# Kernel optimization log

Measured on AMD Instinct MI355X. Metric: run time of the kernel, lower is better.

The kernel has to match this reference:

```python
import jax, jax.numpy as jnp
import numpy as np

B, S, D, H = 8, 128, 256, 8
T = S + 1
HD = D // H  # head_dim = 32
GAMMA = 1.0
NEG_INF = -1e9
LN_EPS = 1e-5


def setup_inputs() -> dict:
    key = jax.random.key(0)
    ks = jax.random.split(key, 16)
    sc = 0.05
    return {
        "desc_embeddings": jax.random.normal(ks[0], (B, S, D), jnp.float32),
        "name_value_embeddings": jax.random.normal(ks[1], (B, T, D), jnp.float32),
        "prior_Q": jax.random.uniform(ks[2], (B, H, S, S), jnp.float32),
        "Wq": jax.random.normal(ks[3], (D, D), jnp.float32) * sc,
        "bq": jnp.zeros((D,), jnp.float32),
        "Wk": jax.random.normal(ks[4], (D, D), jnp.float32) * sc,
        "bk": jnp.zeros((D,), jnp.float32),
        "Wv": jax.random.normal(ks[5], (D, D), jnp.float32) * sc,
        "bv": jnp.zeros((D,), jnp.float32),
        "wa": jax.random.normal(ks[6], (3 * HD,), jnp.float32) * sc,  # attn_proj weight (out=1)
        "ba": jnp.zeros((), jnp.float32),
        "We1": jax.random.normal(ks[7], (2 * D, D), jnp.float32) * sc,
        "be1": jnp.zeros((D,), jnp.float32),
        "ln_g": jnp.ones((D,), jnp.float32),
        "ln_b": jnp.zeros((D,), jnp.float32),
        "We2": jax.random.normal(ks[8], (D, D), jnp.float32) * sc,
        "be2": jnp.zeros((D,), jnp.float32),
    }


def _layer_norm(x, g, b):
    mu = jnp.mean(x, axis=-1, keepdims=True)
    var = jnp.mean(jnp.square(x - mu), axis=-1, keepdims=True)
    return (x - mu) * jax.lax.rsqrt(var + LN_EPS) * g + b


def _heads(x, W, b):  # [B,T,D] -> [B,H,T,HD]
    return (x @ W + b).reshape(B, T, H, HD).transpose(0, 2, 1, 3)


def reference(desc_embeddings, name_value_embeddings, prior_Q,
              Wq, bq, Wk, bk, Wv, bv, wa, ba,
              We1, be1, ln_g, ln_b, We2, be2):
    # structural adjacency (same for every batch element): CLS->Var on, Var->CLS off,
    # Var-Var fully connected without self-loops
    adj = jnp.zeros((T, T), jnp.float32)
    adj = adj.at[1:, 1:].set(1.0 - jnp.eye(S, dtype=jnp.float32))
    adj = adj.at[0, 1:].set(1.0)

    q = _heads(name_value_embeddings, Wq, bq)  # [B,H,T,HD]
    k = _heads(name_value_embeddings, Wk, bk)
    v = _heads(name_value_embeddings, Wv, bv)

    # edge attributes: pairwise concat of desc embeddings, CLS rows/cols use [desc,desc]
    desc = desc_embeddings
    var_edge = jnp.concatenate([
        jnp.broadcast_to(desc[:, :, None, :], (B, S, S, D)),
        jnp.broadcast_to(desc[:, None, :, :], (B, S, S, D)),
    ], axis=-1)  # [B,S,S,2D]
    cls_edge = jnp.concatenate([desc, desc], axis=-1)  # [B,S,2D]
    edge = jnp.zeros((B, T, T, 2 * D), jnp.float32)
    edge = edge.at[:, 1:, 1:].set(var_edge)
    edge = edge.at[:, 0, 1:].set(cls_edge)
    edge = edge.at[:, 1:, 0].set(cls_edge)

    # edge_update MLP: Linear(2D->D) -> LayerNorm -> ReLU -> Linear(D->D)
    h = jax.nn.relu(_layer_norm(edge @ We1 + be1, ln_g, ln_b)) @ We2 + be2  # [B,T,T,D]
    # split into heads, mask by adjacency: [B,H,T,T,HD]
    edge_h = h.reshape(B, T, T, H, HD).transpose(0, 3, 1, 2, 4)
    edge_h = edge_h * adj[None, None, :, :, None]

    # gat_v1 + attn_proj(cat[q_i, k_j, e_ij]) is linear -> decompose to avoid
    # materializing the [B,H,T,T,3*HD] concat
    wa_q, wa_k, wa_e = wa[:HD], wa[HD:2 * HD], wa[2 * HD:]
    logits = (jnp.einsum('bhid,d->bhi', q, wa_q)[:, :, :, None]
              + jnp.einsum('bhjd,d->bhj', k, wa_k)[:, :, None, :]
              + jnp.einsum('bhijd,d->bhij', edge_h, wa_e)
              + ba)  # [B,H,T,T]

    # prior_Q logit-bias injection on Var-Var block
    eps = 1e-6
    p = jnp.clip(prior_Q, eps, 1.0 - eps)
    bias = (jnp.log(p) - jnp.log(1.0 - p)) * GAMMA  # [B,H,S,S]
    logits = logits.at[:, :, 1:, 1:].add(bias)

    # structural mask as pre-softmax -inf
    logits = logits + (adj == 0).astype(logits.dtype)[None, None] * NEG_INF

    attn = jax.nn.softmax(logits, axis=-1)  # [B,H,T,T]
    ctx = jnp.einsum('bhij,bhjd->bhid', attn, v)  # [B,H,T,HD]
    basis_outputs = ctx.transpose(0, 2, 1, 3)  # [B,T,H,HD]
    return basis_outputs, attn
```

## Files before the change

### kernel.cpp

```cpp
#include <hip/hip_runtime.h>
#include <math.h>

#define B 8
#define S 128
#define D 256
#define H 8
#define T 129
#define HD 32
#define BT (B*T)
#define NEG_INF -1000000000.0f
#define LN_EPS 1e-5f

__global__ __launch_bounds__(256) void prep_w(
    const float* __restrict__ Wq, const float* __restrict__ bq,
    const float* __restrict__ Wk, const float* __restrict__ bk,
    const float* __restrict__ We2, const float* __restrict__ be2,
    const float* __restrict__ wa,
    float* __restrict__ Wqk, float* __restrict__ bqk,
    float* __restrict__ W2aT, float* __restrict__ econst)
{
    int id = blockIdx.x * 256 + threadIdx.x;
    if (id < 2048) {
        int c = id >> 3, h = id & 7;
        float s = 0.f;
        #pragma unroll
        for (int d = 0; d < HD; ++d) s = fmaf(Wq[c*D + h*HD + d], wa[d], s);
        Wqk[c*16 + h] = s;
    } else if (id < 4096) {
        int id2 = id - 2048; int c = id2 >> 3, h = id2 & 7;
        float s = 0.f;
        #pragma unroll
        for (int d = 0; d < HD; ++d) s = fmaf(Wk[c*D + h*HD + d], wa[HD + d], s);
        Wqk[c*16 + 8 + h] = s;
    } else if (id < 6144) {
        int id2 = id - 4096; int h = id2 / D, c = id2 % D;
        float s = 0.f;
        #pragma unroll
        for (int d = 0; d < HD; ++d) s = fmaf(We2[c*D + h*HD + d], wa[2*HD + d], s);
        W2aT[h*D + c] = s;
    } else if (id < 6152) {
        int h = id - 6144;
        float s = 0.f;
        #pragma unroll
        for (int d = 0; d < HD; ++d) s = fmaf(bq[h*HD + d], wa[d], s);
        bqk[h] = s;
    } else if (id < 6160) {
        int h = id - 6152;
        float s = 0.f;
        #pragma unroll
        for (int d = 0; d < HD; ++d) s = fmaf(bk[h*HD + d], wa[HD + d], s);
        bqk[8 + h] = s;
    } else if (id < 6168) {
        int h = id - 6160;
        float s = 0.f;
        #pragma unroll
        for (int d = 0; d < HD; ++d) s = fmaf(be2[h*HD + d], wa[2*HD + d], s);
        econst[h] = s;
    }
}

__global__ __launch_bounds__(256) void gemm3(
    const float* __restrict__ nv, const float* __restrict__ desc,
    const float* __restrict__ Wv, const float* __restrict__ bv,
    const float* __restrict__ We1, const float* __restrict__ be1,
    const float* __restrict__ Wqk, const float* __restrict__ bqk,
    float* __restrict__ v, float* __restrict__ U, float* __restrict__ V,
    float* __restrict__ sU, float* __restrict__ sV, float* __restrict__ qdkdT)
{
    const int which = blockIdx.y;
    const int tid = threadIdx.x;
    __shared__ float xs[16][D];
    __shared__ float psum[4][8];

    if (which == 3) {
        if (blockIdx.x >= 65) return;
        const int r0 = blockIdx.x * 16;
        const int r = tid >> 4, c = tid & 15;
        for (int t = tid; t < 16 * D; t += 256) {
            int rr = r0 + (t >> 8);
            xs[t >> 8][t & 255] = (rr < BT) ? nv[rr * D + (t & 255)] : 0.f;
        }
        __syncthreads();
        float acc = 0.f;
        for (int kk = 0; kk < D; kk += 4) {
            float4 x = *(const float4*)&xs[r][kk];
            acc = fmaf(x.x, Wqk[(kk+0)*16 + c], acc);
            acc = fmaf(x.y, Wqk[(kk+1)*16 + c], acc);
            acc = fmaf(x.z, Wqk[(kk+2)*16 + c], acc);
            acc = fmaf(x.w, Wqk[(kk+3)*16 + c], acc);
        }
        const int rr = r0 + r;
        if (rr < BT) qdkdT[c*BT + rr] = acc + bqk[c];
        return;
    }

    const float* X; const float* W; const float* bias; float* out; int rows;
    if (which == 0)      { X = nv;   W = Wv;        bias = bv;  out = v; rows = BT; }
    else if (which == 1) { X = desc; W = We1;       bias = be1; out = U; rows = B*S; }
    else                 { X = desc; W = We1 + D*D; bias = nullptr; out = V; rows = B*S; }

    const int r0 = blockIdx.x * 8;
    if (r0 >= rows) return;

    #pragma unroll
    for (int r = 0; r < 8; ++r) {
        int rr = r0 + r;
        xs[r][tid] = (rr < rows) ? X[rr * D + tid] : 0.f;
    }
    __syncthreads();

    float acc[8] = {0.f,0.f,0.f,0.f,0.f,0.f,0.f,0.f};
    for (int kk = 0; kk < D; kk += 4) {
        float w0 = W[(kk+0)*D + tid];
        float w1 = W[(kk+1)*D + tid];
        float w2 = W[(kk+2)*D + tid];
        float w3 = W[(kk+3)*D + tid];
        #pragma unroll
        for (int r = 0; r < 8; ++r) {
            float4 x = *(const float4*)&xs[r][kk];
            acc[r] = fmaf(x.x, w0, acc[r]);
            acc[r] = fmaf(x.y, w1, acc[r]);
            acc[r] = fmaf(x.z, w2, acc[r]);
            acc[r] = fmaf(x.w, w3, acc[r]);
        }
    }
    const float bb = bias ? bias[tid] : 0.f;
    #pragma unroll
    for (int r = 0; r < 8; ++r) {
        int rr = r0 + r;
        if (rr < rows) out[rr * D + tid] = acc[r] + bb;
    }

    if (which >= 1) {
        const int wv = tid >> 6, ln = tid & 63;
        #pragma unroll
        for (int r = 0; r < 8; ++r) {
            float sps = acc[r] + bb;
            #pragma unroll
            for (int m = 32; m >= 1; m >>= 1) sps += __shfl_xor(sps, m);
            if (ln == 0) psum[wv][r] = sps;
        }
        __syncthreads();
        if (tid < 8) {
            float* dst = (which == 1) ? sU : sV;
            dst[r0 + tid] = psum[0][tid] + psum[1][tid] + psum[2][tid] + psum[3][tid];
        }
    }
}

__device__ __forceinline__ float head_reduce(float* ph, int lane) {
    {
        const bool hi = (lane & 1);
        float k0 = hi ? ph[4] : ph[0], d0 = hi ? ph[0] : ph[4];
        float k1 = hi ? ph[5] : ph[1], d1 = hi ? ph[1] : ph[5];
        float k2 = hi ? ph[6] : ph[2], d2 = hi ? ph[2] : ph[6];
        float k3 = hi ? ph[7] : ph[3], d3 = hi ? ph[3] : ph[7];
        ph[0] = k0 + __shfl_xor(d0, 1);
        ph[1] = k1 + __shfl_xor(d1, 1);
        ph[2] = k2 + __shfl_xor(d2, 1);
        ph[3] = k3 + __shfl_xor(d3, 1);
    }
    {
        const bool hi = (lane & 2);
        float k0 = hi ? ph[2] : ph[0], d0 = hi ? ph[0] : ph[2];
        float k1 = hi ? ph[3] : ph[1], d1 = hi ? ph[1] : ph[3];
        ph[0] = k0 + __shfl_xor(d0, 2);
        ph[1] = k1 + __shfl_xor(d1, 2);
    }
    {
        const bool hi = (lane & 4);
        float k0 = hi ? ph[1] : ph[0], d0 = hi ? ph[0] : ph[1];
        ph[0] = k0 + __shfl_xor(d0, 4);
    }
    float r = ph[0];
    r += __shfl_xor(r, 8);
    r += __shfl_xor(r, 16);
    r += __shfl_xor(r, 32);
    return r;
}

__global__ __launch_bounds__(512, 4) void edge_attn(
    const float* __restrict__ U, const float* __restrict__ V,
    const float* __restrict__ W2aT, const float* __restrict__ econst,
    const float* __restrict__ ln_g, const float* __restrict__ ln_b,
    const float* __restrict__ qdkdT, const float* __restrict__ prior,
    const float* __restrict__ v, const float* __restrict__ ba,
    const float* __restrict__ sU, const float* __restrict__ sV,
    float* __restrict__ out_basis, float* __restrict__ out_attn)
{
    const int bid = blockIdx.x;
    const int b = bid / T, i = bid % T;
    const int tid = threadIdx.x, lane = tid & 63, wid = tid >> 6;
    const int c0 = lane * 4;

    __shared__ float escl[H][132];
    __shared__ float pat[H][132];

    const float4 g4 = *(const float4*)(ln_g + c0);
    const float4 b4 = *(const float4*)(ln_b + c0);
    float4 w[H];
    #pragma unroll
    for (int h = 0; h < H; ++h) w[h] = *(const float4*)(W2aT + h*D + c0);

    float4 u4i = make_float4(0.f, 0.f, 0.f, 0.f);
    float sUi = 0.f;
    if (i >= 1) {
        u4i = *(const float4*)(U + (size_t)(b*S + (i-1))*D + c0);
        sUi = sU[b*S + (i-1)];
    }

    const int hmap = 4*(lane&1) + 2*((lane>>1)&1) + ((lane>>2)&1);
    const float ecl = (lane < 8) ? econst[hmap] : 0.f;

    const int j0 = 1 + wid * 16;
    const float* Vb  = V  + (size_t)(b*S + (j0-1))*D + c0;
    const float* Ub  = U  + (size_t)(b*S + (j0-1))*D + c0;
    const float* sVb = sV + b*S + (j0-1);
    const float* sUb = sU + b*S + (j0-1);

    #pragma unroll 2
    for (int jj = 0; jj < 16; jj += 2) {
        const float4 va  = *(const float4*)(Vb + (size_t)jj*D);
        const float4 vb4 = *(const float4*)(Vb + (size_t)(jj+1)*D);
        float4 ua, ub; float su_a, su_b;
        if (i == 0) {
            ua = *(const float4*)(Ub + (size_t)jj*D);
            ub = *(const float4*)(Ub + (size_t)(jj+1)*D);
            su_a = sUb[jj]; su_b = sUb[jj+1];
        } else { ua = u4i; ub = u4i; su_a = sUi; su_b = sUi; }

        const float mua = (su_a + sVb[jj])   * (1.f/D);
        const float mub = (su_b + sVb[jj+1]) * (1.f/D);

        const float ya0 = ua.x + va.x,  ya1 = ua.y + va.y;
        const float ya2 = ua.z + va.z,  ya3 = ua.w + va.w;
        const float yb0 = ub.x + vb4.x, yb1 = ub.y + vb4.y;
        const float yb2 = ub.z + vb4.z, yb3 = ub.w + vb4.w;

        float s2a = fmaf(ya0, ya0, fmaf(ya1, ya1, fmaf(ya2, ya2, ya3 * ya3)));
        float s2b = fmaf(yb0, yb0, fmaf(yb1, yb1, fmaf(yb2, yb2, yb3 * yb3)));
        #pragma unroll
        for (int m = 32; m >= 1; m >>= 1) {
            s2a += __shfl_xor(s2a, m);
            s2b += __shfl_xor(s2b, m);
        }
        const float vara = fmaf(-mua, mua, s2a * (1.f/D));
        const float varb = fmaf(-mub, mub, s2b * (1.f/D));
        const float rsa = rsqrtf(vara + LN_EPS);
        const float rsb = rsqrtf(varb + LN_EPS);

        const float ta0 = fmaxf(fmaf((ya0 - mua) * rsa, g4.x, b4.x), 0.f);
        const float ta1 = fmaxf(fmaf((ya1 - mua) * rsa, g4.y, b4.y), 0.f);
        const float ta2 = fmaxf(fmaf((ya2 - mua) * rsa, g4.z, b4.z), 0.f);
        const float ta3 = fmaxf(fmaf((ya3 - mua) * rsa, g4.w, b4.w), 0.f);
        const float tb0 = fmaxf(fmaf((yb0 - mub) * rsb, g4.x, b4.x), 0.f);
        const float tb1 = fmaxf(fmaf((yb1 - mub) * rsb, g4.y, b4.y), 0.f);
        const float tb2 = fmaxf(fmaf((yb2 - mub) * rsb, g4.z, b4.z), 0.f);
        const float tb3 = fmaxf(fmaf((yb3 - mub) * rsb, g4.w, b4.w), 0.f);

        float pha[8], phb[8];
        #pragma unroll
        for (int h = 0; h < H; ++h) {
            pha[h] = fmaf(ta0, w[h].x, fmaf(ta1, w[h].y, fmaf(ta2, w[h].z, ta3 * w[h].w)));
            phb[h] = fmaf(tb0, w[h].x, fmaf(tb1, w[h].y, fmaf(tb2, w[h].z, tb3 * w[h].w)));
        }
        const float ra = head_reduce(pha, lane);
        const float rb = head_reduce(phb, lane);
        if (lane < 8) {
            escl[hmap][j0 + jj]     = ra + ecl;
            escl[hmap][j0 + jj + 1] = rb + ecl;
        }
    }
    __syncthreads();

    const int h = wid;
    const int bh = b*H + h;
    const float qdv = qdkdT[h*BT + b*T + i];
    const float ba0 = ba[0];
    const int j1 = 1 + lane, j2 = 65 + lane;
    const bool val1 = !(i >= 1 && j1 == i);
    const bool val2 = !(i >= 1 && j2 == i);
    const float* kT = qdkdT + (8 + h)*BT + b*T;

    float l1 = NEG_INF, l2 = NEG_INF;
    if (val1) {
        l1 = qdv + kT[j1] + escl[h][j1] + ba0;
        if (i >= 1) {
            float pr = prior[((size_t)bh*S + (i-1))*S + (j1-1)];
            pr = fminf(fmaxf(pr, 1e-6f), 1.f - 1e-6f);
            l1 += __logf(pr) - __logf(1.f - pr);
        }
    }
    if (val2) {
        l2 = qdv + kT[j2] + escl[h][j2] + ba0;
        if (i >= 1) {
            float pr = prior[((size_t)bh*S + (i-1))*S + (j2-1)];
            pr = fminf(fmaxf(pr, 1e-6f), 1.f - 1e-6f);
            l2 += __logf(pr) - __logf(1.f - pr);
        }
    }

    float m = fmaxf(l1, l2);
    #pragma unroll
    for (int mm = 32; mm >= 1; mm >>= 1) m = fmaxf(m, __shfl_xor(m, mm));
    const float e1 = val1 ? __expf(l1 - m) : 0.f;
    const float e2 = val2 ? __expf(l2 - m) : 0.f;
    float ssum = e1 + e2;
    #pragma unroll
    for (int mm = 32; mm >= 1; mm >>= 1) ssum += __shfl_xor(ssum, mm);
    const float inv = 1.f / ssum;
    const float a1 = e1 * inv, a2 = e2 * inv;

    float* arow = out_attn + (size_t)(bh*T + i)*T;
    arow[j1] = a1;
    arow[j2] = a2;
    if (lane == 0) arow[0] = 0.f;
    pat[h][j1] = a1;
    pat[h][j2] = a2;
    __syncthreads();

    const int dg = lane & 7;
    const int jg = lane >> 3;
    const float* vbase = v + (size_t)(b*T)*D + h*HD + dg*4;
    float4 acc4 = make_float4(0.f, 0.f, 0.f, 0.f);
    #pragma unroll
    for (int k = 0; k < 16; ++k) {
        const int j = 1 + jg*16 + k;
        const float p = pat[h][j];
        const float4 vv = *(const float4*)(vbase + (size_t)j*D);
        acc4.x = fmaf(p, vv.x, acc4.x);
        acc4.y = fmaf(p, vv.y, acc4.y);
        acc4.z = fmaf(p, vv.z, acc4.z);
        acc4.w = fmaf(p, vv.w, acc4.w);
    }
    #pragma unroll
    for (int mm = 8; mm <= 32; mm <<= 1) {
        acc4.x += __shfl_xor(acc4.x, mm);
        acc4.y += __shfl_xor(acc4.y, mm);
        acc4.z += __shfl_xor(acc4.z, mm);
        acc4.w += __shfl_xor(acc4.w, mm);
    }
    if (jg == 0)
        *(float4*)(out_basis + ((size_t)(b*T + i)*H + h)*HD + dg*4) = acc4;
}

extern "C" void kernel_launch(void* const* d_in, const int* in_sizes, int n_in,
                              void* d_out, int out_size, void* d_ws, size_t ws_size,
                              hipStream_t stream) {
    const float* desc  = (const float*)d_in[0];
    const float* nv    = (const float*)d_in[1];
    const float* prior = (const float*)d_in[2];
    const float* Wq  = (const float*)d_in[3];
    const float* bq  = (const float*)d_in[4];
    const float* Wk  = (const float*)d_in[5];
    const float* bk  = (const float*)d_in[6];
    const float* Wv  = (const float*)d_in[7];
    const float* bv  = (const float*)d_in[8];
    const float* wa  = (const float*)d_in[9];
    const float* ba  = (const float*)d_in[10];
    const float* We1 = (const float*)d_in[11];
    const float* be1 = (const float*)d_in[12];
    const float* lng = (const float*)d_in[13];
    const float* lnb = (const float*)d_in[14];
    const float* We2 = (const float*)d_in[15];
    const float* be2 = (const float*)d_in[16];

    float* ws = (float*)d_ws;
    float* U     = ws; ws += B*S*D;
    float* V     = ws; ws += B*S*D;
    float* v     = ws; ws += B*T*D;
    float* Wqk   = ws; ws += D*16;
    float* bqk   = ws; ws += 16;
    float* W2aT  = ws; ws += H*D;
    float* ec    = ws; ws += H;
    float* qdkdT = ws; ws += 16*BT;
    float* sU    = ws; ws += B*S;
    float* sV    = ws; ws += B*S;

    float* out_basis = (float*)d_out;
    float* out_attn  = out_basis + B*T*H*HD;

    prep_w<<<dim3(25), 256, 0, stream>>>(Wq, bq, Wk, bk, We2, be2, wa,
                                         Wqk, bqk, W2aT, ec);
    gemm3<<<dim3(129, 4), 256, 0, stream>>>(nv, desc, Wv, bv, We1, be1,
                                            Wqk, bqk, v, U, V, sU, sV, qdkdT);
    edge_attn<<<dim3(B*T), 512, 0, stream>>>(U, V, W2aT, ec, lng, lnb,
                                             qdkdT, prior, v, ba, sU, sV,
                                             out_basis, out_attn);
}
```

Measured before the change: 159.9 us.

## Precompute LayerNorm statistics via sum-of-squares decomposition instead of per-pair shuffle reductions

The edge kernel no longer runs a 64-lane shuffle reduction per (i,j) pair to get the LayerNorm variance. The GEMM kernel now also emits per-row sums of squares for U and V, and each edge block computes mean and rstd for all 128 pairs up front from one U·V dot product per pair, storing them in shared memory. The LN affine is folded into a single FMA per element, prior and k loads are hoisted before the edge loop, and the PV accumulation uses an interleaved j index. In exchange each block does an extra 256-wide dot product per pair plus a barrier, and the E[y²]-μ² form may lose some precision.

After: 176.8 us. 1.11x slower.

```diff
diff --git a/kernel.cpp b/kernel.cpp
--- a/kernel.cpp
+++ b/kernel.cpp
@@ -65,12 +65,15 @@
     const float* __restrict__ We1, const float* __restrict__ be1,
     const float* __restrict__ Wqk, const float* __restrict__ bqk,
     float* __restrict__ v, float* __restrict__ U, float* __restrict__ V,
-    float* __restrict__ sU, float* __restrict__ sV, float* __restrict__ qdkdT)
+    float* __restrict__ sU, float* __restrict__ sV,
+    float* __restrict__ s2U, float* __restrict__ s2V,
+    float* __restrict__ qdkdT)
 {
     const int which = blockIdx.y;
     const int tid = threadIdx.x;
     __shared__ float xs[16][D];
     __shared__ float psum[4][8];
+    __shared__ float psq[4][8];
 
     if (which == 3) {
         if (blockIdx.x >= 65) return;
@@ -135,15 +138,22 @@
         const int wv = tid >> 6, ln = tid & 63;
         #pragma unroll
         for (int r = 0; r < 8; ++r) {
-            float sps = acc[r] + bb;
+            float sval = acc[r] + bb;
+            float sps = sval;
+            float sq  = sval * sval;
             #pragma unroll
-            for (int m = 32; m >= 1; m >>= 1) sps += __shfl_xor(sps, m);
-            if (ln == 0) psum[wv][r] = sps;
+            for (int m = 32; m >= 1; m >>= 1) {
+                sps += __shfl_xor(sps, m);
+                sq  += __shfl_xor(sq,  m);
+            }
+            if (ln == 0) { psum[wv][r] = sps; psq[wv][r] = sq; }
         }
         __syncthreads();
         if (tid < 8) {
-            float* dst = (which == 1) ? sU : sV;
-            dst[r0 + tid] = psum[0][tid] + psum[1][tid] + psum[2][tid] + psum[3][tid];
+            float* d1 = (which == 1) ? sU  : sV;
+            float* d2 = (which == 1) ? s2U : s2V;
+            d1[r0 + tid] = psum[0][tid] + psum[1][tid] + psum[2][tid] + psum[3][tid];
+            d2[r0 + tid] = psq[0][tid]  + psq[1][tid]  + psq[2][tid]  + psq[3][tid];
         }
     }
 }
@@ -157,7 +167,7 @@
         float k3 = hi ? ph[7] : ph[3], d3 = hi ? ph[3] : ph[7];
         ph[0] = k0 + __shfl_xor(d0, 1);
         ph[1] = k1 + __shfl_xor(d1, 1);
-        ph[2] = k2 + __shfl_xor(d2, 1);
+        ph[2] = k2 + __shfl_xor(d2, 2 - 1);
         ph[3] = k3 + __shfl_xor(d3, 1);
     }
     {
@@ -186,6 +196,7 @@
     const float* __restrict__ qdkdT, const float* __restrict__ prior,
     const float* __restrict__ v, const float* __restrict__ ba,
     const float* __restrict__ sU, const float* __restrict__ sV,
+    const float* __restrict__ s2U, const float* __restrict__ s2V,
     float* __restrict__ out_basis, float* __restrict__ out_attn)
 {
     const int bid = blockIdx.x;
@@ -195,74 +206,106 @@
 
     __shared__ float escl[H][132];
     __shared__ float pat[H][132];
+    __shared__ float muS[132];
+    __shared__ float rsS[132];
+
+    const int h = wid;
+    const int bh = b*H + h;
+    const int j1 = 1 + lane, j2 = 65 + lane;
+    const float qdv = qdkdT[h*BT + b*T + i];
+    const float ba0 = ba[0];
+    const float* kT = qdkdT + (8 + h)*BT + b*T;
+    const float k1 = kT[j1], k2 = kT[j2];
+    float pr1 = 0.5f, pr2 = 0.5f;
+    if (i >= 1) {
+        pr1 = prior[((size_t)bh*S + (i-1))*S + (j1-1)];
+        pr2 = prior[((size_t)bh*S + (i-1))*S + (j2-1)];
+    }
+
+    {
+        const int jp = (tid >> 2) + 1;
+        const int part = tid & 3;
+        const int urowi = (i >= 1) ? (b*S + i - 1) : (b*S + jp - 1);
+        const float* urow = U + (size_t)urowi * D;
+        const float* vrow = V + (size_t)(b*S + jp - 1) * D;
+        float dotp = 0.f;
+        #pragma unroll
+        for (int c = 0; c < 64; c += 4) {
+            float4 uu = *(const float4*)(urow + part*64 + c);
+            float4 vv = *(const float4*)(vrow + part*64 + c);
+            dotp = fmaf(uu.x, vv.x, dotp);
+            dotp = fmaf(uu.y, vv.y, dotp);
+            dotp = fmaf(uu.z, vv.z, dotp);
+            dotp = fmaf(uu.w, vv.w, dotp);
+        }
+        dotp += __shfl_xor(dotp, 1);
+        dotp += __shfl_xor(dotp, 2);
+        if (part == 0) {
+            const float su  = sU[urowi];
+            const float s2u = s2U[urowi];
+            const float svj  = sV[b*S + jp - 1];
+            const float s2vj = s2V[b*S + jp - 1];
+            const float mu  = (su + svj) * (1.f/D);
+            const float var = fmaf(-mu, mu, (fmaf(2.f, dotp, s2u + s2vj)) * (1.f/D));
+            muS[jp] = mu;
+            rsS[jp] = rsqrtf(var + LN_EPS);
+        }
+    }
 
     const float4 g4 = *(const float4*)(ln_g + c0);
     const float4 b4 = *(const float4*)(ln_b + c0);
     float4 w[H];
     #pragma unroll
-    for (int h = 0; h < H; ++h) w[h] = *(const float4*)(W2aT + h*D + c0);
+    for (int hh = 0; hh < H; ++hh) w[hh] = *(const float4*)(W2aT + hh*D + c0);
 
     float4 u4i = make_float4(0.f, 0.f, 0.f, 0.f);
-    float sUi = 0.f;
-    if (i >= 1) {
-        u4i = *(const float4*)(U + (size_t)(b*S + (i-1))*D + c0);
-        sUi = sU[b*S + (i-1)];
-    }
+    if (i >= 1) u4i = *(const float4*)(U + (size_t)(b*S + (i-1))*D + c0);
 
     const int hmap = 4*(lane&1) + 2*((lane>>1)&1) + ((lane>>2)&1);
     const float ecl = (lane < 8) ? econst[hmap] : 0.f;
 
     const int j0 = 1 + wid * 16;
-    const float* Vb  = V  + (size_t)(b*S + (j0-1))*D + c0;
-    const float* Ub  = U  + (size_t)(b*S + (j0-1))*D + c0;
-    const float* sVb = sV + b*S + (j0-1);
-    const float* sUb = sU + b*S + (j0-1);
+    const float* Vb = V + (size_t)(b*S + (j0-1))*D + c0;
+    const float* Ub = U + (size_t)(b*S + (j0-1))*D + c0;
+
+    __syncthreads();
 
     #pragma unroll 2
     for (int jj = 0; jj < 16; jj += 2) {
         const float4 va  = *(const float4*)(Vb + (size_t)jj*D);
         const float4 vb4 = *(const float4*)(Vb + (size_t)(jj+1)*D);
-        float4 ua, ub; float su_a, su_b;
+        float4 ua, ub;
         if (i == 0) {
             ua = *(const float4*)(Ub + (size_t)jj*D);
             ub = *(const float4*)(Ub + (size_t)(jj+1)*D);
-            su_a = sUb[jj]; su_b = sUb[jj+1];
-        } else { ua = u4i; ub = u4i; su_a = sUi; su_b = sUi; }
-
-        const float mua = (su_a + sVb[jj])   * (1.f/D);
-        const float mub = (su_b + sVb[jj+1]) * (1.f/D);
-
-        const float ya0 = ua.x + va.x,  ya1 = ua.y + va.y;
-        const float ya2 = ua.z + va.z,  ya3 = ua.w + va.w;
-        const float yb0 = ub.x + vb4.x, yb1 = ub.y + vb4.y;
-        const float yb2 = ub.z + vb4.z, yb3 = ub.w + vb4.w;
-
-        float s2a = fmaf(ya0, ya0, fmaf(ya1, ya1, fmaf(ya2, ya2, ya3 * ya3)));
-        float s2b = fmaf(yb0, yb0, fmaf(yb1, yb1, fmaf(yb2, yb2, yb3 * yb3)));
-        #pragma unroll
-        for (int m = 32; m >= 1; m >>= 1) {
-            s2a += __shfl_xor(s2a, m);
-            s2b += __shfl_xor(s2b, m);
-        }
-        const float vara = fmaf(-mua, mua, s2a * (1.f/D));
-        const float varb = fmaf(-mub, mub, s2b * (1.f/D));
-        const float rsa = rsqrtf(vara + LN_EPS);
-        const float rsb = rsqrtf(varb + LN_EPS);
-
-        const float ta0 = fmaxf(fmaf((ya0 - mua) * rsa, g4.x, b4.x), 0.f);
-        const float ta1 = fmaxf(fmaf((ya1 - mua) * rsa, g4.y, b4.y), 0.f);
-        const float ta2 = fmaxf(fmaf((ya2 - mua) * rsa, g4.z, b4.z), 0.f);
-        const float ta3 = fmaxf(fmaf((ya3 - mua) * rsa, g4.w, b4.w), 0.f);
-        const float tb0 = fmaxf(fmaf((yb0 - mub) * rsb, g4.x, b4.x), 0.f);
-        const float tb1 = fmaxf(fmaf((yb1 - mub) * rsb, g4.y, b4.y), 0.f);
-        const float tb2 = fmaxf(fmaf((yb2 - mub) * rsb, g4.z, b4.z), 0.f);
-        const float tb3 = fmaxf(fmaf((yb3 - mub) * rsb, g4.w, b4.w), 0.f);
+        } else { ua = u4i; ub = u4i; }
+
+        const float mua = muS[j0 + jj],  rsa = rsS[j0 + jj];
+        const float mub = muS[j0 + jj + 1], rsb = rsS[j0 + jj + 1];
+
+        const float rga0 = rsa * g4.x, rga1 = rsa * g4.y;
+        const float rga2 = rsa * g4.z, rga3 = rsa * g4.w;
+        const float ofa0 = fmaf(-mua, rga0, b4.x), ofa1 = fmaf(-mua, rga1, b4.y);
+        const float ofa2 = fmaf(-mua, rga2, b4.z), ofa3 = fmaf(-mua, rga3, b4.w);
+        const float rgb0 = rsb * g4.x, rgb1 = rsb * g4.y;
+        const float rgb2 = rsb * g4.z, rgb3 = rsb * g4.w;
+        const float ofb0 = fmaf(-mub, rgb0, b4.x), ofb1 = fmaf(-mub, rgb1, b4.y);
+        const float ofb2 = fmaf(-mub, rgb2, b4.z), ofb3 = fmaf(-mub, rgb3, b4.w);
+
+        const float ta0 = fmaxf(fmaf(ua.x + va.x,  rga0, ofa0), 0.f);
+        const float ta1 = fmaxf(fmaf(ua.y + va.y,  rga1, ofa1), 0.f);
+        const float ta2 = fmaxf(fmaf(ua.z + va.z,  rga2, ofa2), 0.f);
+        const float ta3 = fmaxf(fmaf(ua.w + va.w,  rga3, ofa3), 0.f);
+        const float tb0 = fmaxf(fmaf(ub.x + vb4.x, rgb0, ofb0), 0.f);
+        const float tb1 = fmaxf(fmaf(ub.y + vb4.y, rgb1, ofb1), 0.f);
+        const float tb2 = fmaxf(fmaf(ub.z + vb4.z, rgb2, ofb2), 0.f);
+        const float tb3 = fmaxf(fmaf(ub.w + vb4.w, rgb3, ofb3), 0.f);
 
         float pha[8], phb[8];
         #pragma unroll
-        for (int h = 0; h < H; ++h) {
-            pha[h] = fmaf(ta0, w[h].x, fmaf(ta1, w[h].y, fmaf(ta2, w[h].z, ta3 * w[h].w)));
-            phb[h] = fmaf(tb0, w[h].x, fmaf(tb1, w[h].y, fmaf(tb2, w[h].z, tb3 * w[h].w)));
+        for (int hh = 0; hh < H; ++hh) {
+            pha[hh] = fmaf(ta0, w[hh].x, fmaf(ta1, w[hh].y, fmaf(ta2, w[hh].z, ta3 * w[hh].w)));
+            phb[hh] = fmaf(tb0, w[hh].x, fmaf(tb1, w[hh].y, fmaf(tb2, w[hh].z, tb3 * w[hh].w)));
         }
         const float ra = head_reduce(pha, lane);
         const float rb = head_reduce(phb, lane);
@@ -273,29 +316,21 @@
     }
     __syncthreads();
 
-    const int h = wid;
-    const int bh = b*H + h;
-    const float qdv = qdkdT[h*BT + b*T + i];
-    const float ba0 = ba[0];
-    const int j1 = 1 + lane, j2 = 65 + lane;
     const bool val1 = !(i >= 1 && j1 == i);
     const bool val2 = !(i >= 1 && j2 == i);
-    const float* kT = qdkdT + (8 + h)*BT + b*T;
 
     float l1 = NEG_INF, l2 = NEG_INF;
     if (val1) {
-        l1 = qdv + kT[j1] + escl[h][j1] + ba0;
+        l1 = qdv + k1 + escl[h][j1] + ba0;
         if (i >= 1) {
-            float pr = prior[((size_t)bh*S + (i-1))*S + (j1-1)];
-            pr = fminf(fmaxf(pr, 1e-6f), 1.f - 1e-6f);
+            float pr = fminf(fmaxf(pr1, 1e-6f), 1.f - 1e-6f);
             l1 += __logf(pr) - __logf(1.f - pr);
         }
     }
     if (val2) {
-        l2 = qdv + kT[j2] + escl[h][j2] + ba0;
+        l2 = qdv + k2 + escl[h][j2] + ba0;
         if (i >= 1) {
-            float pr = prior[((size_t)bh*S + (i-1))*S + (j2-1)];
-            pr = fminf(fmaxf(pr, 1e-6f), 1.f - 1e-6f);
+            float pr = fminf(fmaxf(pr2, 1e-6f), 1.f - 1e-6f);
             l2 += __logf(pr) - __logf(1.f - pr);
         }
     }
@@ -325,7 +360,7 @@
     float4 acc4 = make_float4(0.f, 0.f, 0.f, 0.f);
     #pragma unroll
     for (int k = 0; k < 16; ++k) {
-        const int j = 1 + jg*16 + k;
+        const int j = 1 + k*8 + jg;
         const float p = pat[h][j];
         const float4 vv = *(const float4*)(vbase + (size_t)j*D);
         acc4.x = fmaf(p, vv.x, acc4.x);
@@ -376,6 +411,8 @@
     float* qdkdT = ws; ws += 16*BT;
     float* sU    = ws; ws += B*S;
     float* sV    = ws; ws += B*S;
+    float* s2U   = ws; ws += B*S;
+    float* s2V   = ws; ws += B*S;
 
     float* out_basis = (float*)d_out;
     float* out_attn  = out_basis + B*T*H*HD;
@@ -383,8 +420,10 @@
     prep_w<<<dim3(25), 256, 0, stream>>>(Wq, bq, Wk, bk, We2, be2, wa,
                                          Wqk, bqk, W2aT, ec);
     gemm3<<<dim3(129, 4), 256, 0, stream>>>(nv, desc, Wv, bv, We1, be1,
-                                            Wqk, bqk, v, U, V, sU, sV, qdkdT);
+                                            Wqk, bqk, v, U, V,
+                                            sU, sV, s2U, s2V, qdkdT);
     edge_attn<<<dim3(B*T), 512, 0, stream>>>(U, V, W2aT, ec, lng, lnb,
-                                             qdkdT, prior, v, ba, sU, sV,
+                                             qdkdT, prior, v, ba,
+                                             sU, sV, s2U, s2V,
                                              out_basis, out_attn);
 }
```

## Batch four edges per wave with a transpose-style shuffle reduction and prefetch prior loads

Applied to the files above, without the earlier changes.

The edge loop in edge_attn now handles four j values per iteration. The LayerNorm variance and per-head projection sums for all four are folded into one butterfly transpose-reduction, so the wave issues far fewer cross-lane shuffles per edge. The prior, k and q loads for the softmax stage are hoisted to kernel start so their latency overlaps the edge computation. The PV loop now interleaves j indices across lane groups. The cost is more live registers per thread under launch_bounds(512,4), which could cause spills, and more complex lane-select logic.

Result: faster. 146.6 us (-8.3%).

```diff
diff --git a/kernel.cpp b/kernel.cpp
--- a/kernel.cpp
+++ b/kernel.cpp
@@ -146,37 +146,6 @@
             dst[r0 + tid] = psum[0][tid] + psum[1][tid] + psum[2][tid] + psum[3][tid];
         }
     }
-}
-
-__device__ __forceinline__ float head_reduce(float* ph, int lane) {
-    {
-        const bool hi = (lane & 1);
-        float k0 = hi ? ph[4] : ph[0], d0 = hi ? ph[0] : ph[4];
-        float k1 = hi ? ph[5] : ph[1], d1 = hi ? ph[1] : ph[5];
-        float k2 = hi ? ph[6] : ph[2], d2 = hi ? ph[2] : ph[6];
-        float k3 = hi ? ph[7] : ph[3], d3 = hi ? ph[3] : ph[7];
-        ph[0] = k0 + __shfl_xor(d0, 1);
-        ph[1] = k1 + __shfl_xor(d1, 1);
-        ph[2] = k2 + __shfl_xor(d2, 1);
-        ph[3] = k3 + __shfl_xor(d3, 1);
-    }
-    {
-        const bool hi = (lane & 2);
-        float k0 = hi ? ph[2] : ph[0], d0 = hi ? ph[0] : ph[2];
-        float k1 = hi ? ph[3] : ph[1], d1 = hi ? ph[1] : ph[3];
-        ph[0] = k0 + __shfl_xor(d0, 2);
-        ph[1] = k1 + __shfl_xor(d1, 2);
-    }
-    {
-        const bool hi = (lane & 4);
-        float k0 = hi ? ph[1] : ph[0], d0 = hi ? ph[0] : ph[1];
-        ph[0] = k0 + __shfl_xor(d0, 4);
-    }
-    float r = ph[0];
-    r += __shfl_xor(r, 8);
-    r += __shfl_xor(r, 16);
-    r += __shfl_xor(r, 32);
-    return r;
 }
 
 __global__ __launch_bounds__(512, 4) void edge_attn(
@@ -196,106 +165,161 @@
     __shared__ float escl[H][132];
     __shared__ float pat[H][132];
 
+    const int h = wid;
+    const int bh = b*H + h;
+    const int j1 = 1 + lane, j2 = 65 + lane;
+    const float qdv = qdkdT[h*BT + b*T + i];
+    const float ba0 = ba[0];
+    const float* kT = qdkdT + (8 + h)*BT + b*T;
+    const float k1 = kT[j1], k2 = kT[j2];
+    float pr1 = 0.5f, pr2 = 0.5f;
+    if (i >= 1) {
+        pr1 = prior[((size_t)bh*S + (i-1))*S + (j1-1)];
+        pr2 = prior[((size_t)bh*S + (i-1))*S + (j2-1)];
+    }
+
     const float4 g4 = *(const float4*)(ln_g + c0);
     const float4 b4 = *(const float4*)(ln_b + c0);
     float4 w[H];
     #pragma unroll
-    for (int h = 0; h < H; ++h) w[h] = *(const float4*)(W2aT + h*D + c0);
-
+    for (int hh = 0; hh < H; ++hh) w[hh] = *(const float4*)(W2aT + hh*D + c0);
+
+    const bool i0 = (i == 0);
     float4 u4i = make_float4(0.f, 0.f, 0.f, 0.f);
-    float sUi = 0.f;
-    if (i >= 1) {
+    float sUi_s = 0.f;
+    if (!i0) {
         u4i = *(const float4*)(U + (size_t)(b*S + (i-1))*D + c0);
-        sUi = sU[b*S + (i-1)];
-    }
-
+        sUi_s = sU[b*S + (i-1)];
+    }
+
+    const bool bb0 = lane & 1, bb1 = lane & 2, bb2 = lane & 4;
+    const bool bb3 = lane & 8, bb4 = lane & 16;
     const int hmap = 4*(lane&1) + 2*((lane>>1)&1) + ((lane>>2)&1);
-    const float ecl = (lane < 8) ? econst[hmap] : 0.f;
+    const float ech = econst[hmap];
 
     const int j0 = 1 + wid * 16;
-    const float* Vb  = V  + (size_t)(b*S + (j0-1))*D + c0;
-    const float* Ub  = U  + (size_t)(b*S + (j0-1))*D + c0;
+    const float* Vb  = V + (size_t)(b*S + (j0-1))*D + c0;
+    const float* Ub  = U + (size_t)(b*S + (j0-1))*D + c0;
     const float* sVb = sV + b*S + (j0-1);
     const float* sUb = sU + b*S + (j0-1);
 
     #pragma unroll 2
-    for (int jj = 0; jj < 16; jj += 2) {
-        const float4 va  = *(const float4*)(Vb + (size_t)jj*D);
-        const float4 vb4 = *(const float4*)(Vb + (size_t)(jj+1)*D);
-        float4 ua, ub; float su_a, su_b;
-        if (i == 0) {
-            ua = *(const float4*)(Ub + (size_t)jj*D);
-            ub = *(const float4*)(Ub + (size_t)(jj+1)*D);
-            su_a = sUb[jj]; su_b = sUb[jj+1];
-        } else { ua = u4i; ub = u4i; su_a = sUi; su_b = sUi; }
-
-        const float mua = (su_a + sVb[jj])   * (1.f/D);
-        const float mub = (su_b + sVb[jj+1]) * (1.f/D);
-
-        const float ya0 = ua.x + va.x,  ya1 = ua.y + va.y;
-        const float ya2 = ua.z + va.z,  ya3 = ua.w + va.w;
-        const float yb0 = ub.x + vb4.x, yb1 = ub.y + vb4.y;
-        const float yb2 = ub.z + vb4.z, yb3 = ub.w + vb4.w;
-
-        float s2a = fmaf(ya0, ya0, fmaf(ya1, ya1, fmaf(ya2, ya2, ya3 * ya3)));
-        float s2b = fmaf(yb0, yb0, fmaf(yb1, yb1, fmaf(yb2, yb2, yb3 * yb3)));
-        #pragma unroll
-        for (int m = 32; m >= 1; m >>= 1) {
-            s2a += __shfl_xor(s2a, m);
-            s2b += __shfl_xor(s2b, m);
-        }
-        const float vara = fmaf(-mua, mua, s2a * (1.f/D));
-        const float varb = fmaf(-mub, mub, s2b * (1.f/D));
-        const float rsa = rsqrtf(vara + LN_EPS);
-        const float rsb = rsqrtf(varb + LN_EPS);
-
-        const float ta0 = fmaxf(fmaf((ya0 - mua) * rsa, g4.x, b4.x), 0.f);
-        const float ta1 = fmaxf(fmaf((ya1 - mua) * rsa, g4.y, b4.y), 0.f);
-        const float ta2 = fmaxf(fmaf((ya2 - mua) * rsa, g4.z, b4.z), 0.f);
-        const float ta3 = fmaxf(fmaf((ya3 - mua) * rsa, g4.w, b4.w), 0.f);
-        const float tb0 = fmaxf(fmaf((yb0 - mub) * rsb, g4.x, b4.x), 0.f);
-        const float tb1 = fmaxf(fmaf((yb1 - mub) * rsb, g4.y, b4.y), 0.f);
-        const float tb2 = fmaxf(fmaf((yb2 - mub) * rsb, g4.z, b4.z), 0.f);
-        const float tb3 = fmaxf(fmaf((yb3 - mub) * rsb, g4.w, b4.w), 0.f);
-
-        float pha[8], phb[8];
-        #pragma unroll
-        for (int h = 0; h < H; ++h) {
-            pha[h] = fmaf(ta0, w[h].x, fmaf(ta1, w[h].y, fmaf(ta2, w[h].z, ta3 * w[h].w)));
-            phb[h] = fmaf(tb0, w[h].x, fmaf(tb1, w[h].y, fmaf(tb2, w[h].z, tb3 * w[h].w)));
-        }
-        const float ra = head_reduce(pha, lane);
-        const float rb = head_reduce(phb, lane);
-        if (lane < 8) {
-            escl[hmap][j0 + jj]     = ra + ecl;
-            escl[hmap][j0 + jj + 1] = rb + ecl;
+    for (int grp = 0; grp < 4; ++grp) {
+        const int jb = grp * 4;
+        float4 y0 = *(const float4*)(Vb + (size_t)(jb+0)*D);
+        float4 y1 = *(const float4*)(Vb + (size_t)(jb+1)*D);
+        float4 y2 = *(const float4*)(Vb + (size_t)(jb+2)*D);
+        float4 y3 = *(const float4*)(Vb + (size_t)(jb+3)*D);
+        const float4 sv4 = *(const float4*)(sVb + jb);
+        float su0 = sUi_s, su1 = sUi_s, su2 = sUi_s, su3 = sUi_s;
+        float4 u0 = u4i, u1 = u4i, u2 = u4i, u3 = u4i;
+        if (i0) {
+            u0 = *(const float4*)(Ub + (size_t)(jb+0)*D);
+            u1 = *(const float4*)(Ub + (size_t)(jb+1)*D);
+            u2 = *(const float4*)(Ub + (size_t)(jb+2)*D);
+            u3 = *(const float4*)(Ub + (size_t)(jb+3)*D);
+            const float4 su4 = *(const float4*)(sUb + jb);
+            su0 = su4.x; su1 = su4.y; su2 = su4.z; su3 = su4.w;
+        }
+        y0.x += u0.x; y0.y += u0.y; y0.z += u0.z; y0.w += u0.w;
+        y1.x += u1.x; y1.y += u1.y; y1.z += u1.z; y1.w += u1.w;
+        y2.x += u2.x; y2.y += u2.y; y2.z += u2.z; y2.w += u2.w;
+        y3.x += u3.x; y3.y += u3.y; y3.z += u3.z; y3.w += u3.w;
+
+        float s2p0 = fmaf(y0.x,y0.x, fmaf(y0.y,y0.y, fmaf(y0.z,y0.z, y0.w*y0.w)));
+        float s2p1 = fmaf(y1.x,y1.x, fmaf(y1.y,y1.y, fmaf(y1.z,y1.z, y1.w*y1.w)));
+        float s2p2 = fmaf(y2.x,y2.x, fmaf(y2.y,y2.y, fmaf(y2.z,y2.z, y2.w*y2.w)));
+        float s2p3 = fmaf(y3.x,y3.x, fmaf(y3.y,y3.y, fmaf(y3.z,y3.z, y3.w*y3.w)));
+        float a0 = bb0 ? s2p2 : s2p0, d0 = bb0 ? s2p0 : s2p2;
+        float a1 = bb0 ? s2p3 : s2p1, d1 = bb0 ? s2p1 : s2p3;
+        float r0 = a0 + __shfl_xor(d0, 1);
+        float r1 = a1 + __shfl_xor(d1, 1);
+        float a2 = bb1 ? r1 : r0, d2 = bb1 ? r0 : r1;
+        float z = a2 + __shfl_xor(d2, 2);
+        z += __shfl_xor(z, 4);
+        z += __shfl_xor(z, 8);
+        z += __shfl_xor(z, 16);
+        z += __shfl_xor(z, 32);
+        const float mu0 = (su0 + sv4.x) * (1.f/D);
+        const float mu1 = (su1 + sv4.y) * (1.f/D);
+        const float mu2 = (su2 + sv4.z) * (1.f/D);
+        const float mu3 = (su3 + sv4.w) * (1.f/D);
+        const float musel = bb0 ? (bb1 ? mu3 : mu2) : (bb1 ? mu1 : mu0);
+        const float var = fmaf(-musel, musel, z * (1.f/D));
+        const float rsv = rsqrtf(var + LN_EPS);
+        const float rA = __shfl_xor(rsv, 1);
+        const float rB = __shfl_xor(rsv, 2);
+        const float rC = __shfl_xor(rA, 2);
+        const float rs0 = bb0 ? (bb1 ? rC : rA) : (bb1 ? rB : rsv);
+        const float rs1 = bb0 ? (bb1 ? rA : rC) : (bb1 ? rsv : rB);
+        const float rs2 = bb0 ? (bb1 ? rB : rsv) : (bb1 ? rC : rA);
+        const float rs3 = bb0 ? (bb1 ? rsv : rB) : (bb1 ? rA : rC);
+
+        float x0, x1, x2, x3;
+        #define DO_J(YK, RSK, MUK, XOUT)                                          \
+        {                                                                         \
+            const float rg0 = RSK * g4.x, rg1 = RSK * g4.y;                       \
+            const float rg2 = RSK * g4.z, rg3 = RSK * g4.w;                       \
+            const float of0 = fmaf(-MUK, rg0, b4.x), of1 = fmaf(-MUK, rg1, b4.y); \
+            const float of2 = fmaf(-MUK, rg2, b4.z), of3 = fmaf(-MUK, rg3, b4.w); \
+            const float t0 = fmaxf(fmaf(YK.x, rg0, of0), 0.f);                    \
+            const float t1 = fmaxf(fmaf(YK.y, rg1, of1), 0.f);                    \
+            const float t2 = fmaxf(fmaf(YK.z, rg2, of2), 0.f);                    \
+            const float t3 = fmaxf(fmaf(YK.w, rg3, of3), 0.f);                    \
+            float ph0 = fmaf(t0, w[0].x, fmaf(t1, w[0].y, fmaf(t2, w[0].z, t3 * w[0].w))); \
+            float ph1 = fmaf(t0, w[1].x, fmaf(t1, w[1].y, fmaf(t2, w[1].z, t3 * w[1].w))); \
+            float ph2 = fmaf(t0, w[2].x, fmaf(t1, w[2].y, fmaf(t2, w[2].z, t3 * w[2].w))); \
+            float ph3 = fmaf(t0, w[3].x, fmaf(t1, w[3].y, fmaf(t2, w[3].z, t3 * w[3].w))); \
+            float ph4 = fmaf(t0, w[4].x, fmaf(t1, w[4].y, fmaf(t2, w[4].z, t3 * w[4].w))); \
+            float ph5 = fmaf(t0, w[5].x, fmaf(t1, w[5].y, fmaf(t2, w[5].z, t3 * w[5].w))); \
+            float ph6 = fmaf(t0, w[6].x, fmaf(t1, w[6].y, fmaf(t2, w[6].z, t3 * w[6].w))); \
+            float ph7 = fmaf(t0, w[7].x, fmaf(t1, w[7].y, fmaf(t2, w[7].z, t3 * w[7].w))); \
+            float e0 = bb0 ? ph4 : ph0, f0 = bb0 ? ph0 : ph4;                     \
+            float e1 = bb0 ? ph5 : ph1, f1 = bb0 ? ph1 : ph5;                     \
+            float e2 = bb0 ? ph6 : ph2, f2 = bb0 ? ph2 : ph6;                     \
+            float e3 = bb0 ? ph7 : ph3, f3 = bb0 ? ph3 : ph7;                     \
+            float p0 = e0 + __shfl_xor(f0, 1);                                    \
+            float p1 = e1 + __shfl_xor(f1, 1);                                    \
+            float p2 = e2 + __shfl_xor(f2, 1);                                    \
+            float p3 = e3 + __shfl_xor(f3, 1);                                    \
+            float q0 = (bb1 ? p2 : p0) + __shfl_xor(bb1 ? p0 : p2, 2);            \
+            float q1 = (bb1 ? p3 : p1) + __shfl_xor(bb1 ? p1 : p3, 2);            \
+            XOUT = (bb2 ? q1 : q0) + __shfl_xor(bb2 ? q0 : q1, 4);                \
+        }
+        DO_J(y0, rs0, mu0, x0)
+        DO_J(y1, rs1, mu1, x1)
+        DO_J(y2, rs2, mu2, x2)
+        DO_J(y3, rs3, mu3, x3)
+        #undef DO_J
+
+        float tA0 = bb3 ? x2 : x0, sA0 = bb3 ? x0 : x2;
+        float tA1 = bb3 ? x3 : x1, sA1 = bb3 ? x1 : x3;
+        float w0t = tA0 + __shfl_xor(sA0, 8);
+        float w1t = tA1 + __shfl_xor(sA1, 8);
+        float zz = (bb4 ? w1t : w0t) + __shfl_xor(bb4 ? w0t : w1t, 16);
+        zz += __shfl_xor(zz, 32);
+        if (lane < 32) {
+            const int jm = 2*((lane>>3)&1) + ((lane>>4)&1);
+            escl[hmap][j0 + jb + jm] = zz + ech;
         }
     }
     __syncthreads();
 
-    const int h = wid;
-    const int bh = b*H + h;
-    const float qdv = qdkdT[h*BT + b*T + i];
-    const float ba0 = ba[0];
-    const int j1 = 1 + lane, j2 = 65 + lane;
     const bool val1 = !(i >= 1 && j1 == i);
     const bool val2 = !(i >= 1 && j2 == i);
-    const float* kT = qdkdT + (8 + h)*BT + b*T;
 
     float l1 = NEG_INF, l2 = NEG_INF;
     if (val1) {
-        l1 = qdv + kT[j1] + escl[h][j1] + ba0;
+        l1 = qdv + k1 + escl[h][j1] + ba0;
         if (i >= 1) {
-            float pr = prior[((size_t)bh*S + (i-1))*S + (j1-1)];
-            pr = fminf(fmaxf(pr, 1e-6f), 1.f - 1e-6f);
+            float pr = fminf(fmaxf(pr1, 1e-6f), 1.f - 1e-6f);
             l1 += __logf(pr) - __logf(1.f - pr);
         }
     }
     if (val2) {
-        l2 = qdv + kT[j2] + escl[h][j2] + ba0;
+        l2 = qdv + k2 + escl[h][j2] + ba0;
         if (i >= 1) {
-            float pr = prior[((size_t)bh*S + (i-1))*S + (j2-1)];
-            pr = fminf(fmaxf(pr, 1e-6f), 1.f - 1e-6f);
+            float pr = fminf(fmaxf(pr2, 1e-6f), 1.f - 1e-6f);
             l2 += __logf(pr) - __logf(1.f - pr);
         }
     }
@@ -325,7 +349,7 @@
     float4 acc4 = make_float4(0.f, 0.f, 0.f, 0.f);
     #pragma unroll
     for (int k = 0; k < 16; ++k) {
-        const int j = 1 + jg*16 + k;
+        const int j = 1 + k*8 + jg;
         const float p = pat[h][j];
         const float4 vv = *(const float4*)(vbase + (size_t)j*D);
         acc4.x = fmaf(p, vv.x, acc4.x);
```
